# Performance work log

Hardware: AMD Instinct MI355X
Metric: run time of the kernel (lower is better)

Reference implementation:

```python
import jax, jax.numpy as jnp
import numpy as np

E, T, D, N_RBF, N_SBF = 262144, 1048576, 128, 6, 42


def setup_inputs() -> dict:
    key = jax.random.key(0)
    ks = jax.random.split(key, 24)
    s = 0.05
    inp = {
        "m_ji": jax.random.normal(ks[0], (E, D), jnp.float32),
        "e_rbf": jax.random.normal(ks[1], (E, N_RBF), jnp.float32),
        "a_sbf": jax.random.normal(ks[2], (T, N_SBF), jnp.float32),
        "nbr_list": jax.random.randint(ks[3], (E, 2), 0, 65536),
        "kj_idx": jax.random.randint(ks[4], (T,), 0, E),
        "ji_idx": jax.random.randint(ks[5], (T,), 0, E),
        # edge branch params
        "We": jax.random.normal(ks[6], (N_RBF, D), jnp.float32) * s,
        "W_e1": jax.random.normal(ks[7], (D, D), jnp.float32) * s,
        "b_e1": jnp.zeros((D,), jnp.float32),
        "W_e2": jax.random.normal(ks[8], (D, D), jnp.float32) * s,
        "b_e2": jnp.zeros((D,), jnp.float32),
        "W_e3": jax.random.normal(ks[9], (D, D), jnp.float32) * s,
        "b_e3": jnp.zeros((D,), jnp.float32),
        "W_e4": jax.random.normal(ks[10], (D, D), jnp.float32) * s,
        # angle branch params
        "Wa": jax.random.normal(ks[11], (N_SBF, D), jnp.float32) * s,
        "W_a1": jax.random.normal(ks[12], (D, D), jnp.float32) * s,
        "b_a1": jnp.zeros((D,), jnp.float32),
        "W_a2": jax.random.normal(ks[13], (D, D), jnp.float32) * s,
        "b_a2": jnp.zeros((D,), jnp.float32),
        "W_a3": jax.random.normal(ks[14], (D, D), jnp.float32) * s,
        "b_a3": jnp.zeros((D,), jnp.float32),
        "W_a4": jax.random.normal(ks[15], (D, D), jnp.float32) * s,
    }
    return inp


def _mlp(x, W1, b1, W2, b2, W3, b3, W4):
    x = jax.nn.silu(x @ W1 + b1)
    x = jax.nn.silu(x @ W2 + b2)
    x = jax.nn.silu(x @ W3 + b3)
    return x @ W4


def reference(m_ji, e_rbf, a_sbf, nbr_list, kj_idx, ji_idx,
              We, W_e1, b_e1, W_e2, b_e2, W_e3, b_e3, W_e4,
              Wa, W_a1, b_a1, W_a2, b_a2, W_a3, b_a3, W_a4):
    # edge branch: project rbf to embed dim, gate by edge messages  [E, D]
    edge_feats = _mlp((e_rbf @ We) * m_ji, W_e1, b_e1, W_e2, b_e2, W_e3, b_e3, W_e4)
    # angle branch: project sbf, gate by triplet-gathered message sum  [T, D]
    angle_gate = m_ji[kj_idx] + m_ji[ji_idx]
    angle_feats = _mlp((a_sbf @ Wa) * angle_gate, W_a1, b_a1, W_a2, b_a2, W_a3, b_a3, W_a4)
    return (edge_feats, angle_feats)
```

## Files before the change

kernel.cpp:

```cpp
#include <hip/hip_runtime.h>
#include <stdint.h>

#define TPB 512

typedef __attribute__((ext_vector_type(8))) short bf16x8;
typedef __attribute__((ext_vector_type(4))) float f32x4;

static __device__ __forceinline__ unsigned short f2bf_u(float f) {
  __bf16 h = (__bf16)f;
  return __builtin_bit_cast(unsigned short, h);
}
static __device__ __forceinline__ uint32_t pack2bf(float a, float b) {
  return (uint32_t)f2bf_u(a) | ((uint32_t)f2bf_u(b) << 16);
}
static __device__ __forceinline__ float silu_f(float v) {
  float e = __builtin_amdgcn_exp2f(v * -1.44269504088896341f);
  return v * __builtin_amdgcn_rcpf(1.0f + e);
}

static __device__ __forceinline__ void gl_lds16(const void* g, void* l) {
  __builtin_amdgcn_global_load_lds(
      (const __attribute__((address_space(1))) void*)g,
      (__attribute__((address_space(3))) void*)l, 16, 0, 0);
}

static __device__ __forceinline__ void run_mlp(
    char* __restrict__ Wb, char* __restrict__ xb, const char* __restrict__ wt4,
    const float* __restrict__ b1, const float* __restrict__ b2,
    const float* __restrict__ b3, float* __restrict__ outRow, int tid)
{
  const int lane = tid & 63;
  const int wave = tid >> 6;
  const int l15 = lane & 15;
  const int q = lane >> 4;
  const int swz = (lane & 7) << 4;
  const int row = wave * 16 + l15;

  #pragma unroll
  for (int L = 0; L < 4; ++L) {
    __syncthreads();
    {
      const char* src = wt4 + L * 32768;
      #pragma unroll
      for (int c = wave; c < 32; c += 8)
        gl_lds16(src + c * 1024 + lane * 16, Wb + c * 1024);
    }
    __syncthreads();

    f32x4 acc[8];
    #pragma unroll
    for (int ct = 0; ct < 8; ++ct) { f32x4 z = {0.f,0.f,0.f,0.f}; acc[ct] = z; }

    #pragma unroll
    for (int ks = 0; ks < 4; ++ks) {
      const int kb = ks * 64 + q * 16;
      bf16x8 xf = *(const bf16x8*)(xb + ((row * 256 + kb) ^ swz));
      #pragma unroll
      for (int ct = 0; ct < 8; ++ct) {
        bf16x8 wf = *(const bf16x8*)(Wb + (((ct * 16 + l15) * 256 + kb) ^ swz));
        acc[ct] = __builtin_amdgcn_mfma_f32_16x16x32_bf16(wf, xf, acc[ct], 0, 0, 0);
      }
    }

    if (L < 3) {
      const float* bp = (L == 0) ? b1 : (L == 1) ? b2 : b3;
      #pragma unroll
      for (int ct = 0; ct < 8; ++ct) {
        f32x4 bv = *(const f32x4*)(bp + ct * 16 + q * 4);
        float v0 = silu_f(acc[ct][0] + bv[0]);
        float v1 = silu_f(acc[ct][1] + bv[1]);
        float v2 = silu_f(acc[ct][2] + bv[2]);
        float v3 = silu_f(acc[ct][3] + bv[3]);
        uint2 u; u.x = pack2bf(v0, v1); u.y = pack2bf(v2, v3);
        *(uint2*)(xb + ((row * 256 + (ct * 16 + q * 4) * 2) ^ swz)) = u;
      }
    } else {
      #pragma unroll
      for (int ct = 0; ct < 8; ++ct)
        __builtin_nontemporal_store(acc[ct],
            (f32x4*)(outRow + (size_t)row * 128 + ct * 16 + q * 4));
    }
  }
}

__global__ __launch_bounds__(TPB, 4) void edge_kernel(
    const float* __restrict__ m_ji, const float* __restrict__ e_rbf,
    const float* __restrict__ We,
    const float* __restrict__ b1, const float* __restrict__ b2,
    const float* __restrict__ b3,
    const char* __restrict__ wt4, float* __restrict__ out)
{
  __shared__ __align__(16) char Wb[32768];
  __shared__ __align__(16) char xb[32768];
  const int tid = threadIdx.x;
  const int rowbase = blockIdx.x * 128;

  float* WeF = (float*)Wb;
  for (int i = tid; i < 768; i += TPB) WeF[i] = We[i];
  __syncthreads();

  #pragma unroll
  for (int it = 0; it < 8; ++it) {
    const int rowL = it * 16 + (tid >> 5);
    const int col0 = (tid & 31) * 4;
    const int grow = rowbase + rowL;
    f32x4 m = *(const f32x4*)(m_ji + (size_t)grow * 128 + col0);
    const float* ep = e_rbf + (size_t)grow * 6;
    const float e0 = ep[0], e1 = ep[1], e2 = ep[2], e3 = ep[3], e4 = ep[4], e5 = ep[5];
    float s[4];
    #pragma unroll
    for (int j = 0; j < 4; ++j) {
      const int c = col0 + j;
      s[j] = (e0 * WeF[c] + e1 * WeF[128 + c] + e2 * WeF[256 + c]
            + e3 * WeF[384 + c] + e4 * WeF[512 + c] + e5 * WeF[640 + c]) * m[j];
    }
    uint2 u; u.x = pack2bf(s[0], s[1]); u.y = pack2bf(s[2], s[3]);
    *(uint2*)(xb + ((rowL * 256 + col0 * 2) ^ ((rowL & 7) << 4))) = u;
  }

  run_mlp(Wb, xb, wt4, b1, b2, b3, out + (size_t)rowbase * 128, tid);
}

__global__ __launch_bounds__(TPB, 4) void angle_kernel(
    const float* __restrict__ m_ji, const float* __restrict__ a_sbf,
    const int* __restrict__ kj, const int* __restrict__ ji,
    const float* __restrict__ b1, const float* __restrict__ b2,
    const float* __restrict__ b3,
    const char* __restrict__ wt4, const char* __restrict__ waT,
    float* __restrict__ out)
{
  __shared__ __align__(16) char Wb[32768];
  __shared__ __align__(16) char xb[32768];
  const int tid = threadIdx.x;
  const int rowbase = blockIdx.x * 128;
  const int lane = tid & 63, wave = tid >> 6;
  const int l15 = lane & 15, q = lane >> 4;
  const int swz = (lane & 7) << 4;
  const int row = wave * 16 + l15;
  const int gr = rowbase + row;

  const int ikj = kj[gr], iji = ji[gr];

  #pragma unroll
  for (int c = wave; c < 16; c += 8)
    gl_lds16(waT + c * 1024 + lane * 16, Wb + 16384 + c * 1024);

  for (int i = tid; i < 2048; i += TPB) {
    uint2 z; z.x = 0u; z.y = 0u;
    *(uint2*)(Wb + i * 8) = z;
  }
  __syncthreads();
  {
    const float* base = a_sbf + (size_t)rowbase * 42;
    for (int idx = tid; idx < 128 * 42; idx += TPB) {
      const int r = idx / 42;
      const int c = idx - r * 42;
      float v = __builtin_nontemporal_load(base + idx);
      *(unsigned short*)(Wb + ((r * 128 + c * 2) ^ ((r & 7) << 4))) = f2bf_u(v);
    }
  }
  __syncthreads();

  f32x4 acc[8];
  #pragma unroll
  for (int ct = 0; ct < 8; ++ct) { f32x4 z = {0.f,0.f,0.f,0.f}; acc[ct] = z; }

  #pragma unroll
  for (int ks = 0; ks < 2; ++ks) {
    const int kb = ks * 64 + q * 16;
    bf16x8 xf = *(const bf16x8*)(Wb + ((row * 128 + kb) ^ swz));
    #pragma unroll
    for (int ct = 0; ct < 8; ++ct) {
      bf16x8 wf = *(const bf16x8*)(Wb + 16384 + (((ct * 16 + l15) * 128 + kb) ^ swz));
      acc[ct] = __builtin_amdgcn_mfma_f32_16x16x32_bf16(wf, xf, acc[ct], 0, 0, 0);
    }
  }

  {
    const float* pk = m_ji + (size_t)ikj * 128;
    const float* pj = m_ji + (size_t)iji * 128;
    #pragma unroll
    for (int ct = 0; ct < 8; ++ct) {
      const int c0 = ct * 16 + q * 4;
      f32x4 ga = *(const f32x4*)(pk + c0);
      f32x4 gb = *(const f32x4*)(pj + c0);
      uint2 u;
      u.x = pack2bf(acc[ct][0] * (ga[0] + gb[0]), acc[ct][1] * (ga[1] + gb[1]));
      u.y = pack2bf(acc[ct][2] * (ga[2] + gb[2]), acc[ct][3] * (ga[3] + gb[3]));
      *(uint2*)(xb + ((row * 256 + c0 * 2) ^ swz)) = u;
    }
  }

  run_mlp(Wb, xb, wt4, b1, b2, b3, out + (size_t)rowbase * 128, tid);
}

__global__ void prep_kernel(
    const float* __restrict__ W0, const float* __restrict__ W1,
    const float* __restrict__ W2, const float* __restrict__ W3,
    const float* __restrict__ W4, const float* __restrict__ W5,
    const float* __restrict__ W6, const float* __restrict__ W7,
    const float* __restrict__ Wa, char* __restrict__ ws)
{
  const int gid = blockIdx.x * 256 + threadIdx.x;
  if (gid < 8 * 16384) {
    const int m = gid >> 14;
    const int e = gid & 16383;
    const int n = e >> 7, k = e & 127;
    const float* W;
    switch (m) {
      case 0: W = W0; break; case 1: W = W1; break;
      case 2: W = W2; break; case 3: W = W3; break;
      case 4: W = W4; break; case 5: W = W5; break;
      case 6: W = W6; break; default: W = W7; break;
    }
    *(unsigned short*)(ws + m * 32768 + ((n * 256 + k * 2) ^ ((n & 7) << 4))) =
        f2bf_u(W[k * 128 + n]);
  } else {
    const int g = gid - 8 * 16384;
    if (g < 128 * 64) {
      const int n = g >> 6, k = g & 63;
      *(unsigned short*)(ws + 262144 + ((n * 128 + k * 2) ^ ((n & 7) << 4))) =
          (k < 42) ? f2bf_u(Wa[k * 128 + n]) : (unsigned short)0;
    }
  }
}

extern "C" void kernel_launch(void* const* d_in, const int* in_sizes, int n_in,
                              void* d_out, int out_size, void* d_ws, size_t ws_size,
                              hipStream_t stream) {
  (void)in_sizes; (void)n_in; (void)out_size; (void)ws_size;
  const float* m_ji  = (const float*)d_in[0];
  const float* e_rbf = (const float*)d_in[1];
  const float* a_sbf = (const float*)d_in[2];
  const int*   kj    = (const int*)d_in[4];
  const int*   ji    = (const int*)d_in[5];
  const float* We    = (const float*)d_in[6];
  const float* We1   = (const float*)d_in[7];
  const float* be1   = (const float*)d_in[8];
  const float* We2   = (const float*)d_in[9];
  const float* be2   = (const float*)d_in[10];
  const float* We3   = (const float*)d_in[11];
  const float* be3   = (const float*)d_in[12];
  const float* We4   = (const float*)d_in[13];
  const float* Wa    = (const float*)d_in[14];
  const float* Wa1   = (const float*)d_in[15];
  const float* ba1   = (const float*)d_in[16];
  const float* Wa2   = (const float*)d_in[17];
  const float* ba2   = (const float*)d_in[18];
  const float* Wa3   = (const float*)d_in[19];
  const float* ba3   = (const float*)d_in[20];
  const float* Wa4   = (const float*)d_in[21];
  char* ws = (char*)d_ws;
  float* out = (float*)d_out;

  prep_kernel<<<(8 * 16384 + 128 * 64 + 255) / 256, 256, 0, stream>>>(
      We1, We2, We3, We4, Wa1, Wa2, Wa3, Wa4, Wa, ws);
  edge_kernel<<<262144 / 128, TPB, 0, stream>>>(
      m_ji, e_rbf, We, be1, be2, be3, ws, out);
  angle_kernel<<<1048576 / 128, TPB, 0, stream>>>(
      m_ji, a_sbf, kj, ji, ba1, ba2, ba3, ws + 131072, ws + 262144,
      out + (size_t)262144 * 128);
}
```

Before: 618.9 us.

## Make MLP kernels persistent with all four layer weights resident in LDS

Both edge and angle kernels become persistent grids of 256 blocks. Each block loads all four 128x128 bf16 weight matrices once into 128KB of dynamic LDS, pre-arranged in MFMA fragment order, so the per-layer weight reload and the block-wide barriers go away. Each wave then handles its own 16-row tiles independently, prefetching the next tile's gathers and inputs while it runs the current MLP. The rbf and sbf projections now run on MFMA using register-resident weight fragments. The trade is lower occupancy (160KB LDS per block, two blocks per SM bound) and a register-held prefetch.

```diff
diff --git a/kernel.cpp b/kernel.cpp
--- a/kernel.cpp
+++ b/kernel.cpp
@@ -1,10 +1,12 @@
 #include <hip/hip_runtime.h>
 #include <stdint.h>
 
-#define TPB 512
-
 typedef __attribute__((ext_vector_type(8))) short bf16x8;
 typedef __attribute__((ext_vector_type(4))) float f32x4;
+typedef __attribute__((ext_vector_type(8))) unsigned short us8;
+
+#define E_CNT 262144
+#define T_CNT 1048576
 
 static __device__ __forceinline__ unsigned short f2bf_u(float f) {
   __bf16 h = (__bf16)f;
@@ -17,51 +19,32 @@
   float e = __builtin_amdgcn_exp2f(v * -1.44269504088896341f);
   return v * __builtin_amdgcn_rcpf(1.0f + e);
 }
-
 static __device__ __forceinline__ void gl_lds16(const void* g, void* l) {
   __builtin_amdgcn_global_load_lds(
       (const __attribute__((address_space(1))) void*)g,
       (__attribute__((address_space(3))) void*)l, 16, 0, 0);
 }
 
-static __device__ __forceinline__ void run_mlp(
-    char* __restrict__ Wb, char* __restrict__ xb, const char* __restrict__ wt4,
+static __device__ __forceinline__ void mlp4_store(
+    const char* __restrict__ Wb, char* __restrict__ slice,
     const float* __restrict__ b1, const float* __restrict__ b2,
-    const float* __restrict__ b3, float* __restrict__ outRow, int tid)
+    const float* __restrict__ b3, float* __restrict__ outPtr,
+    int l15, int q, int lane, int swz)
 {
-  const int lane = tid & 63;
-  const int wave = tid >> 6;
-  const int l15 = lane & 15;
-  const int q = lane >> 4;
-  const int swz = (lane & 7) << 4;
-  const int row = wave * 16 + l15;
-
   #pragma unroll
   for (int L = 0; L < 4; ++L) {
-    __syncthreads();
-    {
-      const char* src = wt4 + L * 32768;
-      #pragma unroll
-      for (int c = wave; c < 32; c += 8)
-        gl_lds16(src + c * 1024 + lane * 16, Wb + c * 1024);
-    }
-    __syncthreads();
-
     f32x4 acc[8];
     #pragma unroll
     for (int ct = 0; ct < 8; ++ct) { f32x4 z = {0.f,0.f,0.f,0.f}; acc[ct] = z; }
-
     #pragma unroll
     for (int ks = 0; ks < 4; ++ks) {
-      const int kb = ks * 64 + q * 16;
-      bf16x8 xf = *(const bf16x8*)(xb + ((row * 256 + kb) ^ swz));
+      bf16x8 xf = *(const bf16x8*)(slice + ((l15 * 256 + ks * 64 + q * 16) ^ swz));
       #pragma unroll
       for (int ct = 0; ct < 8; ++ct) {
-        bf16x8 wf = *(const bf16x8*)(Wb + (((ct * 16 + l15) * 256 + kb) ^ swz));
+        bf16x8 wf = *(const bf16x8*)(Wb + (((L * 8 + ct) * 4 + ks) << 10) + lane * 16);
         acc[ct] = __builtin_amdgcn_mfma_f32_16x16x32_bf16(wf, xf, acc[ct], 0, 0, 0);
       }
     }
-
     if (L < 3) {
       const float* bp = (L == 0) ? b1 : (L == 1) ? b2 : b3;
       #pragma unroll
@@ -72,126 +55,179 @@
         float v2 = silu_f(acc[ct][2] + bv[2]);
         float v3 = silu_f(acc[ct][3] + bv[3]);
         uint2 u; u.x = pack2bf(v0, v1); u.y = pack2bf(v2, v3);
-        *(uint2*)(xb + ((row * 256 + (ct * 16 + q * 4) * 2) ^ swz)) = u;
+        *(uint2*)(slice + ((l15 * 256 + (ct * 16 + q * 4) * 2) ^ swz)) = u;
       }
     } else {
       #pragma unroll
       for (int ct = 0; ct < 8; ++ct)
-        __builtin_nontemporal_store(acc[ct],
-            (f32x4*)(outRow + (size_t)row * 128 + ct * 16 + q * 4));
+        __builtin_nontemporal_store(acc[ct], (f32x4*)(outPtr + ct * 16));
     }
   }
 }
 
-__global__ __launch_bounds__(TPB, 4) void edge_kernel(
-    const float* __restrict__ m_ji, const float* __restrict__ e_rbf,
-    const float* __restrict__ We,
-    const float* __restrict__ b1, const float* __restrict__ b2,
-    const float* __restrict__ b3,
-    const char* __restrict__ wt4, float* __restrict__ out)
-{
-  __shared__ __align__(16) char Wb[32768];
-  __shared__ __align__(16) char xb[32768];
-  const int tid = threadIdx.x;
-  const int rowbase = blockIdx.x * 128;
-
-  float* WeF = (float*)Wb;
-  for (int i = tid; i < 768; i += TPB) WeF[i] = We[i];
-  __syncthreads();
-
-  #pragma unroll
-  for (int it = 0; it < 8; ++it) {
-    const int rowL = it * 16 + (tid >> 5);
-    const int col0 = (tid & 31) * 4;
-    const int grow = rowbase + rowL;
-    f32x4 m = *(const f32x4*)(m_ji + (size_t)grow * 128 + col0);
-    const float* ep = e_rbf + (size_t)grow * 6;
-    const float e0 = ep[0], e1 = ep[1], e2 = ep[2], e3 = ep[3], e4 = ep[4], e5 = ep[5];
-    float s[4];
-    #pragma unroll
-    for (int j = 0; j < 4; ++j) {
-      const int c = col0 + j;
-      s[j] = (e0 * WeF[c] + e1 * WeF[128 + c] + e2 * WeF[256 + c]
-            + e3 * WeF[384 + c] + e4 * WeF[512 + c] + e5 * WeF[640 + c]) * m[j];
-    }
-    uint2 u; u.x = pack2bf(s[0], s[1]); u.y = pack2bf(s[2], s[3]);
-    *(uint2*)(xb + ((rowL * 256 + col0 * 2) ^ ((rowL & 7) << 4))) = u;
-  }
-
-  run_mlp(Wb, xb, wt4, b1, b2, b3, out + (size_t)rowbase * 128, tid);
-}
-
-__global__ __launch_bounds__(TPB, 4) void angle_kernel(
+__global__ __launch_bounds__(512, 2) void angle_kernel(
     const float* __restrict__ m_ji, const float* __restrict__ a_sbf,
     const int* __restrict__ kj, const int* __restrict__ ji,
     const float* __restrict__ b1, const float* __restrict__ b2,
     const float* __restrict__ b3,
-    const char* __restrict__ wt4, const char* __restrict__ waT,
+    const char* __restrict__ wfrag, const char* __restrict__ waT,
     float* __restrict__ out)
 {
-  __shared__ __align__(16) char Wb[32768];
-  __shared__ __align__(16) char xb[32768];
-  const int tid = threadIdx.x;
-  const int rowbase = blockIdx.x * 128;
-  const int lane = tid & 63, wave = tid >> 6;
+  extern __shared__ char lds[];
+  char* Wb = lds;
+  char* xb = lds + 131072;
+  const int tid = threadIdx.x, lane = tid & 63, wave = tid >> 6;
   const int l15 = lane & 15, q = lane >> 4;
-  const int swz = (lane & 7) << 4;
-  const int row = wave * 16 + l15;
-  const int gr = rowbase + row;
-
-  const int ikj = kj[gr], iji = ji[gr];
-
-  #pragma unroll
-  for (int c = wave; c < 16; c += 8)
-    gl_lds16(waT + c * 1024 + lane * 16, Wb + 16384 + c * 1024);
-
-  for (int i = tid; i < 2048; i += TPB) {
-    uint2 z; z.x = 0u; z.y = 0u;
-    *(uint2*)(Wb + i * 8) = z;
+  const int swz = (l15 & 7) << 4;
+  char* slice = xb + wave * 4096;
+
+  #pragma unroll
+  for (int i = 0; i < 16; ++i)
+    gl_lds16(wfrag + (i * 512 + tid) * 16, Wb + (i * 512 + tid) * 16);
+
+  bf16x8 wa[8][2];
+  #pragma unroll
+  for (int ct = 0; ct < 8; ++ct)
+    #pragma unroll
+    for (int ks = 0; ks < 2; ++ks)
+      wa[ct][ks] = *(const bf16x8*)(waT + ((ct * 2 + ks) * 64 + lane) * 16);
+
+  __syncthreads();
+
+  const int wgid = blockIdx.x * 8 + wave;
+  const int t0 = wgid * 32;
+
+  float as[16];
+  f32x4 pk[8], pj[8];
+
+  auto prefetch = [&](int t) {
+    const int rb = t * 16;
+    const int gr = rb + l15;
+    const int ikj = kj[gr], iji = ji[gr];
+    const float* bk = m_ji + (size_t)ikj * 128 + q * 4;
+    const float* bj = m_ji + (size_t)iji * 128 + q * 4;
+    #pragma unroll
+    for (int ct = 0; ct < 8; ++ct) {
+      pk[ct] = *(const f32x4*)(bk + ct * 16);
+      pj[ct] = *(const f32x4*)(bj + ct * 16);
+    }
+    #pragma unroll
+    for (int i = 0; i < 16; ++i)
+      as[i] = (lane < 42)
+          ? __builtin_nontemporal_load(a_sbf + (size_t)(rb + i) * 42 + lane)
+          : 0.f;
+  };
+
+  prefetch(t0);
+  for (int t = 0; t < 32; ++t) {
+    const int rowbase = (t0 + t) * 16;
+
+    #pragma unroll
+    for (int i = 0; i < 16; ++i)
+      *(unsigned short*)(slice + ((i * 128 + lane * 2) ^ ((i & 7) << 4))) =
+          f2bf_u(as[i]);
+
+    bf16x8 xf0 = *(const bf16x8*)(slice + ((l15 * 128 + q * 16) ^ swz));
+    bf16x8 xf1 = *(const bf16x8*)(slice + ((l15 * 128 + 64 + q * 16) ^ swz));
+
+    f32x4 gs[8];
+    #pragma unroll
+    for (int ct = 0; ct < 8; ++ct) gs[ct] = pk[ct] + pj[ct];
+
+    f32x4 accp[8];
+    #pragma unroll
+    for (int ct = 0; ct < 8; ++ct) {
+      f32x4 z = {0.f,0.f,0.f,0.f};
+      z = __builtin_amdgcn_mfma_f32_16x16x32_bf16(wa[ct][0], xf0, z, 0, 0, 0);
+      z = __builtin_amdgcn_mfma_f32_16x16x32_bf16(wa[ct][1], xf1, z, 0, 0, 0);
+      accp[ct] = z;
+    }
+
+    #pragma unroll
+    for (int ct = 0; ct < 8; ++ct) {
+      uint2 u;
+      u.x = pack2bf(accp[ct][0] * gs[ct][0], accp[ct][1] * gs[ct][1]);
+      u.y = pack2bf(accp[ct][2] * gs[ct][2], accp[ct][3] * gs[ct][3]);
+      *(uint2*)(slice + ((l15 * 256 + (ct * 16 + q * 4) * 2) ^ swz)) = u;
+    }
+
+    if (t < 31) prefetch(t0 + t + 1);
+
+    mlp4_store(Wb, slice, b1, b2, b3,
+               out + (size_t)(rowbase + l15) * 128 + q * 4, l15, q, lane, swz);
   }
+}
+
+__global__ __launch_bounds__(512, 2) void edge_kernel(
+    const float* __restrict__ m_ji, const float* __restrict__ e_rbf,
+    const float* __restrict__ b1, const float* __restrict__ b2,
+    const float* __restrict__ b3,
+    const char* __restrict__ wfrag, const char* __restrict__ weT,
+    float* __restrict__ out)
+{
+  extern __shared__ char lds[];
+  char* Wb = lds;
+  char* xb = lds + 131072;
+  const int tid = threadIdx.x, lane = tid & 63, wave = tid >> 6;
+  const int l15 = lane & 15, q = lane >> 4;
+  const int swz = (l15 & 7) << 4;
+  char* slice = xb + wave * 4096;
+
+  #pragma unroll
+  for (int i = 0; i < 16; ++i)
+    gl_lds16(wfrag + (i * 512 + tid) * 16, Wb + (i * 512 + tid) * 16);
+
+  bf16x8 we[8];
+  #pragma unroll
+  for (int ct = 0; ct < 8; ++ct)
+    we[ct] = *(const bf16x8*)(weT + (ct * 64 + lane) * 16);
+
   __syncthreads();
-  {
-    const float* base = a_sbf + (size_t)rowbase * 42;
-    for (int idx = tid; idx < 128 * 42; idx += TPB) {
-      const int r = idx / 42;
-      const int c = idx - r * 42;
-      float v = __builtin_nontemporal_load(base + idx);
-      *(unsigned short*)(Wb + ((r * 128 + c * 2) ^ ((r & 7) << 4))) = f2bf_u(v);
-    }
+
+  const int wgid = blockIdx.x * 8 + wave;
+  const int t0 = wgid * 8;
+
+  float er[6];
+  f32x4 mr[8];
+  auto prefetch = [&](int t) {
+    const int row = t * 16 + l15;
+    #pragma unroll
+    for (int j = 0; j < 6; ++j) er[j] = e_rbf[(size_t)row * 6 + j];
+    const float* bm = m_ji + (size_t)row * 128 + q * 4;
+    #pragma unroll
+    for (int ct = 0; ct < 8; ++ct) mr[ct] = *(const f32x4*)(bm + ct * 16);
+  };
+
+  prefetch(t0);
+  for (int t = 0; t < 8; ++t) {
+    const int rowbase = (t0 + t) * 16;
+
+    bf16x8 ef;
+    #pragma unroll
+    for (int j = 0; j < 8; ++j) {
+      unsigned short h = (j < 6 && q == 0) ? f2bf_u(er[j]) : (unsigned short)0;
+      ef[j] = (short)h;
+    }
+
+    f32x4 gs[8];
+    #pragma unroll
+    for (int ct = 0; ct < 8; ++ct) gs[ct] = mr[ct];
+
+    #pragma unroll
+    for (int ct = 0; ct < 8; ++ct) {
+      f32x4 z = {0.f,0.f,0.f,0.f};
+      z = __builtin_amdgcn_mfma_f32_16x16x32_bf16(we[ct], ef, z, 0, 0, 0);
+      uint2 u;
+      u.x = pack2bf(z[0] * gs[ct][0], z[1] * gs[ct][1]);
+      u.y = pack2bf(z[2] * gs[ct][2], z[3] * gs[ct][3]);
+      *(uint2*)(slice + ((l15 * 256 + (ct * 16 + q * 4) * 2) ^ swz)) = u;
+    }
+
+    if (t < 7) prefetch(t0 + t + 1);
+
+    mlp4_store(Wb, slice, b1, b2, b3,
+               out + (size_t)(rowbase + l15) * 128 + q * 4, l15, q, lane, swz);
   }
-  __syncthreads();
-
-  f32x4 acc[8];
-  #pragma unroll
-  for (int ct = 0; ct < 8; ++ct) { f32x4 z = {0.f,0.f,0.f,0.f}; acc[ct] = z; }
-
-  #pragma unroll
-  for (int ks = 0; ks < 2; ++ks) {
-    const int kb = ks * 64 + q * 16;
-    bf16x8 xf = *(const bf16x8*)(Wb + ((row * 128 + kb) ^ swz));
-    #pragma unroll
-    for (int ct = 0; ct < 8; ++ct) {
-      bf16x8 wf = *(const bf16x8*)(Wb + 16384 + (((ct * 16 + l15) * 128 + kb) ^ swz));
-      acc[ct] = __builtin_amdgcn_mfma_f32_16x16x32_bf16(wf, xf, acc[ct], 0, 0, 0);
-    }
-  }
-
-  {
-    const float* pk = m_ji + (size_t)ikj * 128;
-    const float* pj = m_ji + (size_t)iji * 128;
-    #pragma unroll
-    for (int ct = 0; ct < 8; ++ct) {
-      const int c0 = ct * 16 + q * 4;
-      f32x4 ga = *(const f32x4*)(pk + c0);
-      f32x4 gb = *(const f32x4*)(pj + c0);
-      uint2 u;
-      u.x = pack2bf(acc[ct][0] * (ga[0] + gb[0]), acc[ct][1] * (ga[1] + gb[1]));
-      u.y = pack2bf(acc[ct][2] * (ga[2] + gb[2]), acc[ct][3] * (ga[3] + gb[3]));
-      *(uint2*)(xb + ((row * 256 + c0 * 2) ^ swz)) = u;
-    }
-  }
-
-  run_mlp(Wb, xb, wt4, b1, b2, b3, out + (size_t)rowbase * 128, tid);
 }
 
 __global__ void prep_kernel(
@@ -199,29 +235,52 @@
     const float* __restrict__ W2, const float* __restrict__ W3,
     const float* __restrict__ W4, const float* __restrict__ W5,
     const float* __restrict__ W6, const float* __restrict__ W7,
-    const float* __restrict__ Wa, char* __restrict__ ws)
+    const float* __restrict__ Wa, const float* __restrict__ We,
+    char* __restrict__ ws)
 {
   const int gid = blockIdx.x * 256 + threadIdx.x;
-  if (gid < 8 * 16384) {
-    const int m = gid >> 14;
-    const int e = gid & 16383;
-    const int n = e >> 7, k = e & 127;
+  const int lane = gid & 63;
+  const int l15 = lane & 15, q = lane >> 4;
+  if (gid < 16384) {
+    const int mat = gid >> 11;
+    const int ctks = (gid & 2047) >> 6;
+    const int n = (ctks >> 2) * 16 + l15;
+    const int k0 = (ctks & 3) * 32 + q * 8;
     const float* W;
-    switch (m) {
+    switch (mat) {
       case 0: W = W0; break; case 1: W = W1; break;
       case 2: W = W2; break; case 3: W = W3; break;
       case 4: W = W4; break; case 5: W = W5; break;
       case 6: W = W6; break; default: W = W7; break;
     }
-    *(unsigned short*)(ws + m * 32768 + ((n * 256 + k * 2) ^ ((n & 7) << 4))) =
-        f2bf_u(W[k * 128 + n]);
-  } else {
-    const int g = gid - 8 * 16384;
-    if (g < 128 * 64) {
-      const int n = g >> 6, k = g & 63;
-      *(unsigned short*)(ws + 262144 + ((n * 128 + k * 2) ^ ((n & 7) << 4))) =
-          (k < 42) ? f2bf_u(Wa[k * 128 + n]) : (unsigned short)0;
-    }
+    us8 v;
+    #pragma unroll
+    for (int j = 0; j < 8; ++j) v[j] = f2bf_u(W[(size_t)(k0 + j) * 128 + n]);
+    *(us8*)(ws + mat * 32768 + ctks * 1024 + lane * 16) = v;
+  } else if (gid < 17408) {
+    const int g = gid - 16384;
+    const int ctks = g >> 6;
+    const int n = (ctks >> 1) * 16 + l15;
+    const int k0 = (ctks & 1) * 32 + q * 8;
+    us8 v;
+    #pragma unroll
+    for (int j = 0; j < 8; ++j) {
+      const int k = k0 + j;
+      v[j] = (k < 42) ? f2bf_u(Wa[(size_t)k * 128 + n]) : (unsigned short)0;
+    }
+    *(us8*)(ws + 262144 + ctks * 1024 + lane * 16) = v;
+  } else if (gid < 17920) {
+    const int g = gid - 17408;
+    const int ct = g >> 6;
+    const int n = ct * 16 + l15;
+    const int k0 = q * 8;
+    us8 v;
+    #pragma unroll
+    for (int j = 0; j < 8; ++j) {
+      const int k = k0 + j;
+      v[j] = (k < 6) ? f2bf_u(We[(size_t)k * 128 + n]) : (unsigned short)0;
+    }
+    *(us8*)(ws + 278528 + ct * 1024 + lane * 16) = v;
   }
 }
 
@@ -253,11 +312,16 @@
   char* ws = (char*)d_ws;
   float* out = (float*)d_out;
 
-  prep_kernel<<<(8 * 16384 + 128 * 64 + 255) / 256, 256, 0, stream>>>(
-      We1, We2, We3, We4, Wa1, Wa2, Wa3, Wa4, Wa, ws);
-  edge_kernel<<<262144 / 128, TPB, 0, stream>>>(
-      m_ji, e_rbf, We, be1, be2, be3, ws, out);
-  angle_kernel<<<1048576 / 128, TPB, 0, stream>>>(
+  hipFuncSetAttribute((const void*)edge_kernel,
+                      hipFuncAttributeMaxDynamicSharedMemorySize, 163840);
+  hipFuncSetAttribute((const void*)angle_kernel,
+                      hipFuncAttributeMaxDynamicSharedMemorySize, 163840);
+
+  prep_kernel<<<70, 256, 0, stream>>>(
+      We1, We2, We3, We4, Wa1, Wa2, Wa3, Wa4, Wa, We, ws);
+  edge_kernel<<<256, 512, 163840, stream>>>(
+      m_ji, e_rbf, be1, be2, be3, ws, ws + 278528, out);
+  angle_kernel<<<256, 512, 163840, stream>>>(
       m_ji, a_sbf, kj, ji, ba1, ba2, ba3, ws + 131072, ws + 262144,
       out + (size_t)262144 * 128);
 }
```

Measured after the change: 1.202 ms. 94.2% more time.
